# Kernel tuning notes

Measured on AMD Instinct MI355X. Metric: run time of the kernel, lower is better.

## Reference

```python
import jax, jax.numpy as jnp
import numpy as np

EPS = 1e-8
MARGIN = 0.2
LAMBDA_SM_LSE = 6.0   # i2t attention smooth (opt.lambda_softmax_lse)
LAMBDA_SM_AVG = 9.0   # t2i attention smooth (opt.lambda_softmax_avg)
LAMBDA_LSE = 6.0      # LogSumExp aggregation temperature
NEG = -1e9


def _l2norm(x, axis):
    return x / (jnp.sqrt(jnp.sum(x * x, axis=axis, keepdims=True)) + EPS)


def _cos(a, b):
    # cosine over last axis, torch-style: w12 / clamp(|a||b|, eps)
    w12 = jnp.sum(a * b, axis=-1)
    w1 = jnp.sqrt(jnp.sum(a * a, axis=-1))
    w2 = jnp.sqrt(jnp.sum(b * b, axis=-1))
    return w12 / jnp.maximum(w1 * w2, EPS)


def _forward(im, s, s_l):
    B, R, D = im.shape
    W = s.shape[1]
    wmask = jnp.arange(W)[None, :] < s_l[:, None]          # (Bc, W) valid words
    s = s * wmask[:, :, None]                              # emulate ragged slice s[j,:len_j]

    # ---------------- i2t: query=image regions, context=caption words ----------
    # attn[i,j,w,r] = <s[j,w], im[i,r]>
    A = jnp.einsum('jwd,ird->ijwr', s, im)
    A = jax.nn.leaky_relu(A, 0.1)
    A = _l2norm(A, axis=3)                                 # clipped_l2norm over regions
    logits = jnp.swapaxes(A, 2, 3) * LAMBDA_SM_LSE         # (i,j,r,w), softmax over words
    logits = jnp.where(wmask[None, :, None, :], logits, NEG)
    attn_i2t = jax.nn.softmax(logits, axis=-1)
    wc_t = jnp.einsum('ijrw,jwd->ijrd', attn_i2t, s)       # weighted caption ctx per region
    sim1 = _cos(im[:, None, :, :], wc_t)                   # (i,j,r)
    score1 = jnp.log(jnp.sum(jnp.exp(LAMBDA_LSE * sim1), axis=2)) / LAMBDA_LSE  # (i,j)
    attn_t_full = jnp.mean(wc_t, axis=2)                   # (i,j,d)
    idx = jnp.arange(B)
    attn_t = attn_t_full[idx, idx]                         # (B,d) diagonal

    # ---------------- t2i: query=caption words, context=image regions ----------
    # attn[i,j,r,w] = <im[i,r], s[j,w]>
    Bm = jnp.einsum('ird,jwd->ijrw', im, s)
    Bm = jax.nn.leaky_relu(Bm, 0.1)
    Bm = Bm * wmask[None, :, None, :]                      # padded-word cols excluded from norm
    Bm = _l2norm(Bm, axis=3)                               # clipped_l2norm over words
    logits2 = jnp.swapaxes(Bm, 2, 3) * LAMBDA_SM_AVG       # (i,j,w,r), softmax over regions
    attn_t2i = jax.nn.softmax(logits2, axis=-1)
    wc_i = jnp.einsum('ijwr,ird->ijwd', attn_t2i, im)      # weighted image ctx per word
    sim2 = _cos(s[None, :, :, :], wc_i)                    # (i,j,w)
    e2 = jnp.where(wmask[None, :, :], jnp.exp(LAMBDA_LSE * sim2), 0.0)
    score2 = jnp.log(jnp.sum(e2, axis=2)) / LAMBDA_LSE     # masked LogSumExp over words
    wsum = jnp.sum(wc_i * wmask[None, :, :, None], axis=2)
    attn_i_full = wsum / s_l[None, :, None].astype(wc_i.dtype)  # masked mean over words
    attn_i = attn_i_full[idx, idx]                         # (B,d)

    # ---------------- hinge loss over (B,B) score matrix -----------------------
    scores = 0.5 * (score1 + score2)
    diag = jnp.diagonal(scores)
    cost_s = jnp.maximum(MARGIN + scores - diag[:, None], 0.0)
    cost_im = jnp.maximum(MARGIN + scores - diag[None, :], 0.0)
    eye = jnp.eye(B, dtype=bool)
    cost_s = jnp.where(eye, 0.0, cost_s)
    cost_im = jnp.where(eye, 0.0, cost_im)
    # max_violation=True
    loss = jnp.sum(jnp.max(cost_s, axis=1)) + jnp.sum(jnp.max(cost_im, axis=0))
    return loss, attn_t, attn_i


def setup_inputs() -> dict:
    key = jax.random.key(0)
    k1, k2, k3 = jax.random.split(key, 3)
    B, R, W, D = 64, 36, 40, 1024
    im = jax.random.normal(k1, (B, R, D), dtype=jnp.float32)
    s = jax.random.normal(k2, (B, W, D), dtype=jnp.float32)
    s_l = jax.random.randint(k3, (B,), 10, W + 1)
    return {"im": im, "s": s, "s_l": s_l}


def reference(im, s, s_l):
    return _forward(im, s, s_l)
```

## Files before the change

kernel.cpp:

```cpp
#include <hip/hip_runtime.h>
#include <math.h>

#define Bn 64
#define Rr 36
#define Ww 40
#define Dd 1024
#define GM 2304
#define GN 2560
#define GLP 44
#define EPSf 1e-8f

typedef unsigned short u16;
typedef __attribute__((ext_vector_type(8))) short bf16x8;
typedef __attribute__((ext_vector_type(4))) float f32x4;

struct alignas(8) U16x4 { u16 x, y, z, w; };

__device__ inline u16 f2bf(float x) {
    unsigned int u = __float_as_uint(x);
    u += 0x7FFFu + ((u >> 16) & 1u);
    return (u16)(u >> 16);
}
__device__ inline float bf2f(u16 h) {
    return __uint_as_float(((unsigned int)h) << 16);
}

__device__ __forceinline__ void gl_lds16(const u16* g, u16* l) {
    __builtin_amdgcn_global_load_lds(
        (const __attribute__((address_space(1))) void*)g,
        (__attribute__((address_space(3))) void*)l, 16, 0, 0);
}

__global__ __launch_bounds__(256) void convert_kernel(const float* __restrict__ im,
                                                      const float* __restrict__ s,
                                                      const int* __restrict__ s_l,
                                                      u16* __restrict__ Ab,
                                                      u16* __restrict__ Bb) {
    const int nA4 = GM * Dd / 4;
    const int nB4 = GN * Dd / 4;
    int idx = blockIdx.x * 256 + threadIdx.x;
    if (idx < nA4) {
        float4 v = *(const float4*)(im + (size_t)idx * 4);
        U16x4 o = {f2bf(v.x), f2bf(v.y), f2bf(v.z), f2bf(v.w)};
        *(U16x4*)(Ab + (size_t)idx * 4) = o;
    } else if (idx < nA4 + nB4) {
        int i2 = idx - nA4;
        int f = i2 * 4;
        int row = f >> 10;
        int j = row / Ww, w = row - j * Ww;
        U16x4 o = {0, 0, 0, 0};
        if (w < s_l[j]) {
            float4 v = *(const float4*)(s + (size_t)f);
            o.x = f2bf(v.x); o.y = f2bf(v.y); o.z = f2bf(v.z); o.w = f2bf(v.w);
        }
        *(U16x4*)(Bb + (size_t)i2 * 4) = o;
    }
}

__global__ __launch_bounds__(256) void gram_mfma_kernel(const u16* __restrict__ Ab,
                                                        const u16* __restrict__ Bb,
                                                        float* __restrict__ SS,
                                                        float* __restrict__ II) {
    int b = blockIdx.x;
    bool isS = b < Bn;
    int idx = isS ? b : b - Bn;
    int n = isS ? Ww : Rr;
    const u16* base = isS ? (Bb + (size_t)idx * Ww * Dd) : (Ab + (size_t)idx * Rr * Dd);
    float* outp = isS ? (SS + (size_t)idx * Ww * Ww) : (II + (size_t)idx * Rr * Rr);
    int t = threadIdx.x, lane = t & 63, wid = t >> 6;
    int frow = lane & 15, fk = (lane >> 4) * 8;
    __shared__ float red[3][64][37];

    f32x4 acc[3][3];
    for (int m = 0; m < 3; ++m)
        for (int p = 0; p < 3; ++p) acc[m][p] = (f32x4){0.f, 0.f, 0.f, 0.f};

    for (int ks = 0; ks < 8; ++ks) {
        int k0 = wid * 256 + ks * 32;
        bf16x8 f[3];
        for (int m = 0; m < 3; ++m)
            f[m] = *(const bf16x8*)(base + (size_t)(m * 16 + frow) * Dd + k0 + fk);
        for (int m = 0; m < 3; ++m)
            for (int p = 0; p < 3; ++p)
                acc[m][p] = __builtin_amdgcn_mfma_f32_16x16x32_bf16(f[m], f[p], acc[m][p], 0, 0, 0);
    }
    if (wid) {
        for (int m = 0; m < 3; ++m)
            for (int p = 0; p < 3; ++p)
                for (int q = 0; q < 4; ++q)
                    red[wid - 1][lane][(m * 3 + p) * 4 + q] = acc[m][p][q];
    }
    __syncthreads();
    if (wid == 0) {
        for (int wv = 0; wv < 3; ++wv)
            for (int m = 0; m < 3; ++m)
                for (int p = 0; p < 3; ++p)
                    for (int q = 0; q < 4; ++q)
                        acc[m][p][q] += red[wv][lane][(m * 3 + p) * 4 + q];
        int crow = (lane >> 4) * 4, ccol = lane & 15;
        for (int m = 0; m < 3; ++m)
            for (int p = 0; p < 3; ++p)
                for (int q = 0; q < 4; ++q) {
                    int row = m * 16 + crow + q;
                    int col = p * 16 + ccol;
                    if (row < n && col < n) outp[row * n + col] = acc[m][p][q];
                }
    }
}

template <bool GB>
__global__ __launch_bounds__(256) void gemm_mfma_kernel(const u16* __restrict__ Ab,
                                                        const u16* __restrict__ Bb,
                                                        void* __restrict__ Gv) {
    __shared__ __align__(16) u16 As[2][64][64];
    __shared__ __align__(16) u16 Bs[2][128][64];
    int bn = blockIdx.x;
    int bm = blockIdx.y;
    int t = threadIdx.x;
    int lane = t & 63, wid = t >> 6;
    int wr = wid >> 1, wc = wid & 1;

    int lrow8 = lane >> 3;
    int sslot = (lane & 7) ^ lrow8;
    const u16* ga = Ab + ((size_t)(bm * 64 + wid * 16) + lrow8) * Dd + sslot * 8;
    const u16* gb = Bb + ((size_t)(bn * 128 + wid * 32) + lrow8) * Dd + sslot * 8;

    f32x4 acc[2][4];
    for (int m = 0; m < 2; ++m)
        for (int n = 0; n < 4; ++n) acc[m][n] = (f32x4){0.f, 0.f, 0.f, 0.f};

    int frow = lane & 15;
    int cgr = lane >> 4;

#define STAGE(BI, KK) do { \
        gl_lds16(ga + (KK), &As[BI][wid * 16][0]); \
        gl_lds16(ga + (size_t)8 * Dd + (KK), &As[BI][wid * 16 + 8][0]); \
        gl_lds16(gb + (KK), &Bs[BI][wid * 32][0]); \
        gl_lds16(gb + (size_t)8 * Dd + (KK), &Bs[BI][wid * 32 + 8][0]); \
        gl_lds16(gb + (size_t)16 * Dd + (KK), &Bs[BI][wid * 32 + 16][0]); \
        gl_lds16(gb + (size_t)24 * Dd + (KK), &Bs[BI][wid * 32 + 24][0]); \
    } while (0)

    STAGE(0, 0);
    for (int step = 0; step < 16; ++step) {
        int cur = step & 1;
        __syncthreads();
        if (step < 15) STAGE(cur ^ 1, (step + 1) * 64);
        bf16x8 af[2][2], bf[4][2];
#pragma unroll
        for (int m = 0; m < 2; ++m) {
            int row = wr * 32 + m * 16 + frow;
#pragma unroll
            for (int ks = 0; ks < 2; ++ks) {
                int slot = (ks * 4 + cgr) ^ (row & 7);
                af[m][ks] = *(const bf16x8*)&As[cur][row][slot * 8];
            }
        }
#pragma unroll
        for (int n = 0; n < 4; ++n) {
            int row = wc * 64 + n * 16 + frow;
#pragma unroll
            for (int ks = 0; ks < 2; ++ks) {
                int slot = (ks * 4 + cgr) ^ (row & 7);
                bf[n][ks] = *(const bf16x8*)&Bs[cur][row][slot * 8];
            }
        }
#pragma unroll
        for (int ks = 0; ks < 2; ++ks)
#pragma unroll
            for (int m = 0; m < 2; ++m)
#pragma unroll
                for (int n = 0; n < 4; ++n)
                    acc[m][n] = __builtin_amdgcn_mfma_f32_16x16x32_bf16(af[m][ks], bf[n][ks], acc[m][n], 0, 0, 0);
    }
#undef STAGE

    int crow0 = bm * 64 + wr * 32 + (lane >> 4) * 4;
    int ccol0 = bn * 128 + wc * 64 + (lane & 15);
    for (int m = 0; m < 2; ++m)
        for (int q = 0; q < 4; ++q) {
            int row = crow0 + m * 16 + q;
            for (int n = 0; n < 4; ++n) {
                float v = acc[m][n][q];
                size_t off = (size_t)row * GN + ccol0 + n * 16;
                if (GB) ((u16*)Gv)[off] = f2bf(v);
                else ((float*)Gv)[off] = v;
            }
        }
}

template <bool GB>
__global__ __launch_bounds__(128) void pair_kernel(const void* __restrict__ Gv,
                                                   const float* __restrict__ SS,
                                                   const float* __restrict__ II,
                                                   const int* __restrict__ s_l,
                                                   float* __restrict__ score1,
                                                   float* __restrict__ score2,
                                                   float* __restrict__ dAp,
                                                   float* __restrict__ dBp) {
    int j = blockIdx.x, i = blockIdx.y;
    int t = threadIdx.x, lane = t & 63, wid = t >> 6;
    __shared__ __align__(16) u16 glb[Rr * GLP];
    __shared__ __align__(16) u16 attA[Ww * Rr];
    __shared__ __align__(16) u16 attB[Rr * Ww];
    __shared__ float invA[Ww], invB[Rr], sA[Rr], sB[Ww];
    __shared__ float qpA[360], qpB[360];
    int L = s_l[j];
    float iid = 0.f, ssd = 0.f;

    if (wid == 0) {
        if (lane < Rr) {
            iid = II[(size_t)i * Rr * Rr + lane * (Rr + 1)];
            if (GB) {
                const u16* gp = (const u16*)Gv + (size_t)(i * Rr + lane) * GN + j * Ww;
#pragma unroll
                for (int q = 0; q < 10; ++q)
                    *(uint2*)&glb[lane * GLP + q * 4] = *(const uint2*)(gp + q * 4);
            } else {
                const float* gp = (const float*)Gv + (size_t)(i * Rr + lane) * GN + j * Ww;
#pragma unroll
                for (int q = 0; q < 10; ++q) {
                    float4 v = *(const float4*)(gp + q * 4);
                    U16x4 h = {f2bf(v.x), f2bf(v.y), f2bf(v.z), f2bf(v.w)};
                    *(uint2*)&glb[lane * GLP + q * 4] = *(const uint2*)&h;
                }
            }
            float sum = 0.f;
#pragma unroll 8
            for (int w = 0; w < Ww; ++w) {
                float x = bf2f(glb[lane * GLP + w]);
                x = x < 0.f ? 0.1f * x : x;
                sum += x * x;
            }
            invB[lane] = 9.f / (sqrtf(sum) + EPSf);
        }
    } else {
        if (lane < Ww) ssd = SS[(size_t)j * Ww * Ww + lane * (Ww + 1)];
    }
    __syncthreads();
    if (wid == 1 && lane < Ww) {
        float sum = 0.f;
#pragma unroll 6
        for (int r = 0; r < Rr; ++r) {
            float x = bf2f(glb[r * GLP + lane]);
            x = x < 0.f ? 0.1f * x : x;
            sum += x * x;
        }
        invA[lane] = 6.f / (sqrtf(sum) + EPSf);
    }
    __syncthreads();
    if (wid == 0) {
        float dot = 0.f, myinv = 0.f;
        if (lane < Rr) {
            float ssum = 0.f;
#pragma unroll 8
            for (int w = 0; w < Ww; ++w) {
                float e = 0.f;
                if (w < L) {
                    float gx = bf2f(glb[lane * GLP + w]);
                    float x = gx < 0.f ? 0.1f * gx : gx;
                    e = __expf(x * invA[w]);
                    dot += e * gx;
                }
                attA[w * Rr + lane] = f2bf(e);
                ssum += e;
            }
            myinv = 1.f / ssum;
            dot *= myinv;
            sA[lane] = myinv;
        }
#pragma unroll
        for (int rd = 0; rd < 2; ++rd) {
            int job = lane + rd * 64;
            if (job < 90) {
                int wg = job / 9, rg = job - (job / 9) * 9;
                float a4[4][4];
#pragma unroll
                for (int x = 0; x < 4; ++x)
#pragma unroll
                    for (int y = 0; y < 4; ++y) a4[x][y] = 0.f;
                const float* SSp = SS + (size_t)j * Ww * Ww + wg * 4;
#pragma unroll 4
                for (int w = 0; w < Ww; ++w) {
                    ushort4 a16 = *(const ushort4*)&attA[w * Rr + rg * 4];
                    float4 sv = *(const float4*)(SSp + w * Ww);
                    float av0 = bf2f(a16.x), av1 = bf2f(a16.y), av2 = bf2f(a16.z), av3 = bf2f(a16.w);
                    a4[0][0] += av0 * sv.x; a4[0][1] += av0 * sv.y; a4[0][2] += av0 * sv.z; a4[0][3] += av0 * sv.w;
                    a4[1][0] += av1 * sv.x; a4[1][1] += av1 * sv.y; a4[1][2] += av1 * sv.z; a4[1][3] += av1 * sv.w;
                    a4[2][0] += av2 * sv.x; a4[2][1] += av2 * sv.y; a4[2][2] += av2 * sv.z; a4[2][3] += av2 * sv.w;
                    a4[3][0] += av3 * sv.x; a4[3][1] += av3 * sv.y; a4[3][2] += av3 * sv.z; a4[3][3] += av3 * sv.w;
                }
                float qv0 = 0.f, qv1 = 0.f, qv2 = 0.f, qv3 = 0.f;
#pragma unroll
                for (int wj = 0; wj < 4; ++wj) {
                    ushort4 b16 = *(const ushort4*)&attA[(wg * 4 + wj) * Rr + rg * 4];
                    qv0 += bf2f(b16.x) * a4[0][wj];
                    qv1 += bf2f(b16.y) * a4[1][wj];
                    qv2 += bf2f(b16.z) * a4[2][wj];
                    qv3 += bf2f(b16.w) * a4[3][wj];
                }
                qpA[(rg * 4 + 0) * 10 + wg] = qv0;
                qpA[(rg * 4 + 1) * 10 + wg] = qv1;
                qpA[(rg * 4 + 2) * 10 + wg] = qv2;
                qpA[(rg * 4 + 3) * 10 + wg] = qv3;
            }
        }
        float e1 = 0.f;
        if (lane < Rr) {
            float q = 0.f;
#pragma unroll
            for (int wg = 0; wg < 10; ++wg) q += qpA[lane * 10 + wg];
            q *= myinv * myinv;
            float s1 = dot / fmaxf(sqrtf(iid) * sqrtf(fmaxf(q, 0.f)), EPSf);
            e1 = __expf(6.f * s1);
        }
#pragma unroll
        for (int off = 1; off < 64; off <<= 1) e1 += __shfl_xor(e1, off);
        if (lane == 0) score1[i * Bn + j] = __logf(e1) * (1.f / 6.f);
        if (i == j && lane < Ww) {
            float sum = 0.f;
#pragma unroll 6
            for (int r = 0; r < Rr; ++r) sum += bf2f(attA[lane * Rr + r]) * sA[r];
            dAp[i * Ww + lane] = sum * (1.f / (float)Rr);
        }
    } else {
        float dot = 0.f, myinv = 0.f;
        if (lane < Ww) {
            float ssum = 0.f;
#pragma unroll 6
            for (int r = 0; r < Rr; ++r) {
                float gx = bf2f(glb[r * GLP + lane]);
                float x = gx < 0.f ? 0.1f * gx : gx;
                float e = __expf(x * invB[r]);
                dot += e * gx;
                attB[r * Ww + lane] = f2bf(e);
                ssum += e;
            }
            myinv = 1.f / ssum;
            dot *= myinv;
            sB[lane] = myinv;
        }
#pragma unroll
        for (int rd = 0; rd < 2; ++rd) {
            int job = lane + rd * 64;
            if (job < 90) {
                int rg = job / 10, wg = job - (job / 10) * 10;
                float a4[4][4];
#pragma unroll
                for (int x = 0; x < 4; ++x)
#pragma unroll
                    for (int y = 0; y < 4; ++y) a4[x][y] = 0.f;
                const float* IIp = II + (size_t)i * Rr * Rr + rg * 4;
#pragma unroll 4
                for (int r = 0; r < Rr; ++r) {
                    ushort4 b16 = *(const ushort4*)&attB[r * Ww + wg * 4];
                    float4 iv = *(const float4*)(IIp + r * Rr);
                    float bv0 = bf2f(b16.x), bv1 = bf2f(b16.y), bv2 = bf2f(b16.z), bv3 = bf2f(b16.w);
                    a4[0][0] += bv0 * iv.x; a4[0][1] += bv0 * iv.y; a4[0][2] += bv0 * iv.z; a4[0][3] += bv0 * iv.w;
                    a4[1][0] += bv1 * iv.x; a4[1][1] += bv1 * iv.y; a4[1][2] += bv1 * iv.z; a4[1][3] += bv1 * iv.w;
                    a4[2][0] += bv2 * iv.x; a4[2][1] += bv2 * iv.y; a4[2][2] += bv2 * iv.z; a4[2][3] += bv2 * iv.w;
                    a4[3][0] += bv3 * iv.x; a4[3][1] += bv3 * iv.y; a4[3][2] += bv3 * iv.z; a4[3][3] += bv3 * iv.w;
                }
                float qv0 = 0.f, qv1 = 0.f, qv2 = 0.f, qv3 = 0.f;
#pragma unroll
                for (int rj = 0; rj < 4; ++rj) {
                    ushort4 b2 = *(const ushort4*)&attB[(rg * 4 + rj) * Ww + wg * 4];
                    qv0 += bf2f(b2.x) * a4[0][rj];
                    qv1 += bf2f(b2.y) * a4[1][rj];
                    qv2 += bf2f(b2.z) * a4[2][rj];
                    qv3 += bf2f(b2.w) * a4[3][rj];
                }
                qpB[(wg * 4 + 0) * 9 + rg] = qv0;
                qpB[(wg * 4 + 1) * 9 + rg] = qv1;
                qpB[(wg * 4 + 2) * 9 + rg] = qv2;
                qpB[(wg * 4 + 3) * 9 + rg] = qv3;
            }
        }
        float e2 = 0.f;
        if (lane < Ww) {
            float q = 0.f;
#pragma unroll
            for (int rg = 0; rg < 9; ++rg) q += qpB[lane * 9 + rg];
            q *= myinv * myinv;
            float s2 = dot / fmaxf(sqrtf(ssd) * sqrtf(fmaxf(q, 0.f)), EPSf);
            e2 = (lane < L) ? __expf(6.f * s2) : 0.f;
        }
#pragma unroll
        for (int off = 1; off < 64; off <<= 1) e2 += __shfl_xor(e2, off);
        if (lane == 0) score2[i * Bn + j] = __logf(e2) * (1.f / 6.f);
        if (i == j && lane < Rr) {
            float sum = 0.f;
            for (int w = 0; w < L; ++w) sum += bf2f(attB[lane * Ww + w]) * sB[w];
            dBp[i * Rr + lane] = sum / (float)L;
        }
    }
}

__global__ __launch_bounds__(256) void diag_out_kernel(const u16* __restrict__ Ab,
                                                       const u16* __restrict__ Bb,
                                                       const int* __restrict__ s_l,
                                                       const float* __restrict__ dA,
                                                       const float* __restrict__ dB,
                                                       const float* __restrict__ score1,
                                                       const float* __restrict__ score2,
                                                       float* __restrict__ out) {
    int t = threadIdx.x;
    if (blockIdx.y == 4) {
        if (blockIdx.x != 0) return;
        __shared__ float sc[Bn][Bn + 1];
        for (int idx = t; idx < Bn * Bn; idx += 256)
            sc[idx >> 6][idx & 63] = 0.5f * (score1[idx] + score2[idx]);
        __syncthreads();
        if (t < 64) {
            float dt = sc[t][t];
            float rowmax = 0.f, colmax = 0.f;
            for (int k = 0; k < Bn; ++k) {
                if (k != t) {
                    rowmax = fmaxf(rowmax, 0.2f + sc[t][k] - dt);
                    colmax = fmaxf(colmax, 0.2f + sc[k][t] - dt);
                }
            }
            float v = rowmax + colmax;
            for (int off = 32; off; off >>= 1) v += __shfl_down(v, off);
            if (t == 0) out[0] = v;
        }
        return;
    }
    int i = blockIdx.x;
    int d = blockIdx.y * 256 + t;
    int L = s_l[i];
    __shared__ float aw[Ww], br[Rr];
    if (t < Ww) aw[t] = dA[i * Ww + t];
    if (t >= 64 && t < 64 + Rr) br[t - 64] = dB[i * Rr + (t - 64)];
    __syncthreads();
    float acc1 = 0.f;
    for (int w = 0; w < L; ++w) acc1 += aw[w] * bf2f(Bb[((size_t)i * Ww + w) * Dd + d]);
    out[1 + (size_t)i * Dd + d] = acc1;
    float acc2 = 0.f;
    for (int r = 0; r < Rr; ++r) acc2 += br[r] * bf2f(Ab[((size_t)i * Rr + r) * Dd + d]);
    out[1 + (size_t)Bn * Dd + (size_t)i * Dd + d] = acc2;
}

extern "C" void kernel_launch(void* const* d_in, const int* in_sizes, int n_in,
                              void* d_out, int out_size, void* d_ws, size_t ws_size,
                              hipStream_t stream) {
    const float* im = (const float*)d_in[0];
    const float* s = (const float*)d_in[1];
    const int* s_l = (const int*)d_in[2];
    float* out = (float*)d_out;

    const size_t nAb = (size_t)GM * Dd;
    const size_t nBb = (size_t)GN * Dd;
    u16* Ab = (u16*)d_ws;
    u16* Bb = Ab + nAb;
    float* SS = (float*)(Bb + nBb);
    float* II = SS + (size_t)Bn * Ww * Ww;
    float* score1 = II + (size_t)Bn * Rr * Rr;
    float* score2 = score1 + Bn * Bn;
    float* dA = score2 + Bn * Bn;
    float* dB = dA + Bn * Ww;
    void* G = (void*)(dB + Bn * Rr);
    size_t base_bytes = (char*)G - (char*)d_ws;
    bool g_fp32 = (ws_size >= base_bytes + (size_t)GM * GN * 4);

    int nconv = (GM * Dd + GN * Dd) / 4;
    convert_kernel<<<(nconv + 255) / 256, 256, 0, stream>>>(im, s, s_l, Ab, Bb);
    gram_mfma_kernel<<<2 * Bn, 256, 0, stream>>>(Ab, Bb, SS, II);

    dim3 ggrid(GN / 128, GM / 64);
    dim3 pgrid(Bn, Bn);
    if (g_fp32) {
        gemm_mfma_kernel<false><<<ggrid, 256, 0, stream>>>(Ab, Bb, G);
        pair_kernel<false><<<pgrid, 128, 0, stream>>>(G, SS, II, s_l, score1, score2, dA, dB);
    } else {
        gemm_mfma_kernel<true><<<ggrid, 256, 0, stream>>>(Ab, Bb, G);
        pair_kernel<true><<<pgrid, 128, 0, stream>>>(G, SS, II, s_l, score1, score2, dA, dB);
    }

    dim3 dgrid(Bn, 5);
    diag_out_kernel<<<dgrid, 256, 0, stream>>>(Ab, Bb, s_l, dA, dB, score1, score2, out);
}
```

Baseline: 79.37 us.

## Fuse pairwise GEMM into per-pair attention kernel and merge convert with Gram

Measured after the change: 147.4 us. +85.7%, slower.

```diff
diff --git a/kernel.cpp b/kernel.cpp
--- a/kernel.cpp
+++ b/kernel.cpp
@@ -7,7 +7,8 @@
 #define Dd 1024
 #define GM 2304
 #define GN 2560
-#define GLP 44
+#define GP 41
+#define NCONV 4864
 #define EPSf 1e-8f
 
 typedef unsigned short u16;
@@ -25,61 +26,65 @@
     return __uint_as_float(((unsigned int)h) << 16);
 }
 
-__device__ __forceinline__ void gl_lds16(const u16* g, u16* l) {
-    __builtin_amdgcn_global_load_lds(
-        (const __attribute__((address_space(1))) void*)g,
-        (__attribute__((address_space(3))) void*)l, 16, 0, 0);
-}
-
-__global__ __launch_bounds__(256) void convert_kernel(const float* __restrict__ im,
-                                                      const float* __restrict__ s,
-                                                      const int* __restrict__ s_l,
-                                                      u16* __restrict__ Ab,
-                                                      u16* __restrict__ Bb) {
-    const int nA4 = GM * Dd / 4;
-    const int nB4 = GN * Dd / 4;
-    int idx = blockIdx.x * 256 + threadIdx.x;
-    if (idx < nA4) {
-        float4 v = *(const float4*)(im + (size_t)idx * 4);
-        U16x4 o = {f2bf(v.x), f2bf(v.y), f2bf(v.z), f2bf(v.w)};
-        *(U16x4*)(Ab + (size_t)idx * 4) = o;
-    } else if (idx < nA4 + nB4) {
-        int i2 = idx - nA4;
-        int f = i2 * 4;
-        int row = f >> 10;
-        int j = row / Ww, w = row - j * Ww;
-        U16x4 o = {0, 0, 0, 0};
-        if (w < s_l[j]) {
-            float4 v = *(const float4*)(s + (size_t)f);
-            o.x = f2bf(v.x); o.y = f2bf(v.y); o.z = f2bf(v.z); o.w = f2bf(v.w);
-        }
-        *(U16x4*)(Bb + (size_t)i2 * 4) = o;
-    }
-}
-
-__global__ __launch_bounds__(256) void gram_mfma_kernel(const u16* __restrict__ Ab,
-                                                        const u16* __restrict__ Bb,
-                                                        float* __restrict__ SS,
-                                                        float* __restrict__ II) {
-    int b = blockIdx.x;
-    bool isS = b < Bn;
-    int idx = isS ? b : b - Bn;
+__global__ __launch_bounds__(256) void prep_kernel(const float* __restrict__ im,
+                                                   const float* __restrict__ s,
+                                                   const int* __restrict__ s_l,
+                                                   u16* __restrict__ Ab,
+                                                   u16* __restrict__ Bb,
+                                                   float* __restrict__ SS,
+                                                   float* __restrict__ II) {
+    __shared__ float red[3][64][37];
+    int b = blockIdx.x, t = threadIdx.x;
+    if (b < NCONV) {
+        const int nA4 = GM * Dd / 4;
+        int idx = b * 256 + t;
+        if (idx < nA4) {
+            float4 v = *(const float4*)(im + (size_t)idx * 4);
+            U16x4 o = {f2bf(v.x), f2bf(v.y), f2bf(v.z), f2bf(v.w)};
+            *(U16x4*)(Ab + (size_t)idx * 4) = o;
+        } else {
+            int i2 = idx - nA4;
+            int f = i2 * 4;
+            int row = f >> 10;
+            int j = row / Ww, w = row - j * Ww;
+            U16x4 o = {0, 0, 0, 0};
+            if (w < s_l[j]) {
+                float4 v = *(const float4*)(s + (size_t)f);
+                o.x = f2bf(v.x); o.y = f2bf(v.y); o.z = f2bf(v.z); o.w = f2bf(v.w);
+            }
+            *(U16x4*)(Bb + (size_t)i2 * 4) = o;
+        }
+        return;
+    }
+    int gb = b - NCONV;
+    bool isS = gb < Bn;
+    int idx = isS ? gb : gb - Bn;
     int n = isS ? Ww : Rr;
-    const u16* base = isS ? (Bb + (size_t)idx * Ww * Dd) : (Ab + (size_t)idx * Rr * Dd);
+    const float* basef = isS ? (s + (size_t)idx * Ww * Dd) : (im + (size_t)idx * Rr * Dd);
     float* outp = isS ? (SS + (size_t)idx * Ww * Ww) : (II + (size_t)idx * Rr * Rr);
-    int t = threadIdx.x, lane = t & 63, wid = t >> 6;
+    int lane = t & 63, wid = t >> 6;
     int frow = lane & 15, fk = (lane >> 4) * 8;
-    __shared__ float red[3][64][37];
 
     f32x4 acc[3][3];
     for (int m = 0; m < 3; ++m)
         for (int p = 0; p < 3; ++p) acc[m][p] = (f32x4){0.f, 0.f, 0.f, 0.f};
 
     for (int ks = 0; ks < 8; ++ks) {
-        int k0 = wid * 256 + ks * 32;
+        int k0 = wid * 256 + ks * 32 + fk;
         bf16x8 f[3];
-        for (int m = 0; m < 3; ++m)
-            f[m] = *(const bf16x8*)(base + (size_t)(m * 16 + frow) * Dd + k0 + fk);
+        for (int m = 0; m < 3; ++m) {
+            int rr = m * 16 + frow;
+            if (rr >= n) rr = n - 1;
+            const float* p = basef + (size_t)rr * Dd + k0;
+            float4 v0 = *(const float4*)p;
+            float4 v1 = *(const float4*)(p + 4);
+            bf16x8 fv;
+            fv[0] = (short)f2bf(v0.x); fv[1] = (short)f2bf(v0.y);
+            fv[2] = (short)f2bf(v0.z); fv[3] = (short)f2bf(v0.w);
+            fv[4] = (short)f2bf(v1.x); fv[5] = (short)f2bf(v1.y);
+            fv[6] = (short)f2bf(v1.z); fv[7] = (short)f2bf(v1.w);
+            f[m] = fv;
+        }
         for (int m = 0; m < 3; ++m)
             for (int p = 0; p < 3; ++p)
                 acc[m][p] = __builtin_amdgcn_mfma_f32_16x16x32_bf16(f[m], f[p], acc[m][p], 0, 0, 0);
@@ -108,203 +113,188 @@
     }
 }
 
-template <bool GB>
-__global__ __launch_bounds__(256) void gemm_mfma_kernel(const u16* __restrict__ Ab,
-                                                        const u16* __restrict__ Bb,
-                                                        void* __restrict__ Gv) {
-    __shared__ __align__(16) u16 As[2][64][64];
-    __shared__ __align__(16) u16 Bs[2][128][64];
-    int bn = blockIdx.x;
-    int bm = blockIdx.y;
-    int t = threadIdx.x;
-    int lane = t & 63, wid = t >> 6;
-    int wr = wid >> 1, wc = wid & 1;
-
-    int lrow8 = lane >> 3;
-    int sslot = (lane & 7) ^ lrow8;
-    const u16* ga = Ab + ((size_t)(bm * 64 + wid * 16) + lrow8) * Dd + sslot * 8;
-    const u16* gb = Bb + ((size_t)(bn * 128 + wid * 32) + lrow8) * Dd + sslot * 8;
-
-    f32x4 acc[2][4];
-    for (int m = 0; m < 2; ++m)
-        for (int n = 0; n < 4; ++n) acc[m][n] = (f32x4){0.f, 0.f, 0.f, 0.f};
-
-    int frow = lane & 15;
-    int cgr = lane >> 4;
-
-#define STAGE(BI, KK) do { \
-        gl_lds16(ga + (KK), &As[BI][wid * 16][0]); \
-        gl_lds16(ga + (size_t)8 * Dd + (KK), &As[BI][wid * 16 + 8][0]); \
-        gl_lds16(gb + (KK), &Bs[BI][wid * 32][0]); \
-        gl_lds16(gb + (size_t)8 * Dd + (KK), &Bs[BI][wid * 32 + 8][0]); \
-        gl_lds16(gb + (size_t)16 * Dd + (KK), &Bs[BI][wid * 32 + 16][0]); \
-        gl_lds16(gb + (size_t)24 * Dd + (KK), &Bs[BI][wid * 32 + 24][0]); \
-    } while (0)
-
-    STAGE(0, 0);
-    for (int step = 0; step < 16; ++step) {
-        int cur = step & 1;
-        __syncthreads();
-        if (step < 15) STAGE(cur ^ 1, (step + 1) * 64);
-        bf16x8 af[2][2], bf[4][2];
-#pragma unroll
-        for (int m = 0; m < 2; ++m) {
-            int row = wr * 32 + m * 16 + frow;
-#pragma unroll
-            for (int ks = 0; ks < 2; ++ks) {
-                int slot = (ks * 4 + cgr) ^ (row & 7);
-                af[m][ks] = *(const bf16x8*)&As[cur][row][slot * 8];
-            }
-        }
-#pragma unroll
-        for (int n = 0; n < 4; ++n) {
-            int row = wc * 64 + n * 16 + frow;
-#pragma unroll
-            for (int ks = 0; ks < 2; ++ks) {
-                int slot = (ks * 4 + cgr) ^ (row & 7);
-                bf[n][ks] = *(const bf16x8*)&Bs[cur][row][slot * 8];
-            }
-        }
-#pragma unroll
-        for (int ks = 0; ks < 2; ++ks)
-#pragma unroll
-            for (int m = 0; m < 2; ++m)
-#pragma unroll
-                for (int n = 0; n < 4; ++n)
-                    acc[m][n] = __builtin_amdgcn_mfma_f32_16x16x32_bf16(af[m][ks], bf[n][ks], acc[m][n], 0, 0, 0);
-    }
-#undef STAGE
-
-    int crow0 = bm * 64 + wr * 32 + (lane >> 4) * 4;
-    int ccol0 = bn * 128 + wc * 64 + (lane & 15);
-    for (int m = 0; m < 2; ++m)
-        for (int q = 0; q < 4; ++q) {
-            int row = crow0 + m * 16 + q;
-            for (int n = 0; n < 4; ++n) {
-                float v = acc[m][n][q];
-                size_t off = (size_t)row * GN + ccol0 + n * 16;
-                if (GB) ((u16*)Gv)[off] = f2bf(v);
-                else ((float*)Gv)[off] = v;
-            }
-        }
-}
-
-template <bool GB>
-__global__ __launch_bounds__(128) void pair_kernel(const void* __restrict__ Gv,
-                                                   const float* __restrict__ SS,
-                                                   const float* __restrict__ II,
-                                                   const int* __restrict__ s_l,
-                                                   float* __restrict__ score1,
-                                                   float* __restrict__ score2,
-                                                   float* __restrict__ dAp,
-                                                   float* __restrict__ dBp) {
+__global__ __launch_bounds__(256) void fused_kernel(const u16* __restrict__ Ab,
+                                                    const u16* __restrict__ Bb,
+                                                    const float* __restrict__ SS,
+                                                    const float* __restrict__ II,
+                                                    const int* __restrict__ s_l,
+                                                    float* __restrict__ score1,
+                                                    float* __restrict__ score2,
+                                                    float* __restrict__ dAp,
+                                                    float* __restrict__ dBp) {
     int j = blockIdx.x, i = blockIdx.y;
     int t = threadIdx.x, lane = t & 63, wid = t >> 6;
-    __shared__ __align__(16) u16 glb[Rr * GLP];
+    __shared__ __align__(16) float gacc[Rr * GP];
     __shared__ __align__(16) u16 attA[Ww * Rr];
     __shared__ __align__(16) u16 attB[Rr * Ww];
     __shared__ float invA[Ww], invB[Rr], sA[Rr], sB[Ww];
-    __shared__ float qpA[360], qpB[360];
+    __shared__ __align__(16) float qpA[360], qpB[360];
     int L = s_l[j];
+
     float iid = 0.f, ssd = 0.f;
-
-    if (wid == 0) {
-        if (lane < Rr) {
-            iid = II[(size_t)i * Rr * Rr + lane * (Rr + 1)];
-            if (GB) {
-                const u16* gp = (const u16*)Gv + (size_t)(i * Rr + lane) * GN + j * Ww;
-#pragma unroll
-                for (int q = 0; q < 10; ++q)
-                    *(uint2*)&glb[lane * GLP + q * 4] = *(const uint2*)(gp + q * 4);
-            } else {
-                const float* gp = (const float*)Gv + (size_t)(i * Rr + lane) * GN + j * Ww;
-#pragma unroll
-                for (int q = 0; q < 10; ++q) {
-                    float4 v = *(const float4*)(gp + q * 4);
-                    U16x4 h = {f2bf(v.x), f2bf(v.y), f2bf(v.z), f2bf(v.w)};
-                    *(uint2*)&glb[lane * GLP + q * 4] = *(const uint2*)&h;
-                }
-            }
-            float sum = 0.f;
-#pragma unroll 8
-            for (int w = 0; w < Ww; ++w) {
-                float x = bf2f(glb[lane * GLP + w]);
-                x = x < 0.f ? 0.1f * x : x;
-                sum += x * x;
-            }
-            invB[lane] = 9.f / (sqrtf(sum) + EPSf);
-        }
-    } else {
-        if (lane < Ww) ssd = SS[(size_t)j * Ww * Ww + lane * (Ww + 1)];
-    }
-    __syncthreads();
+    if (wid == 0 && lane < Rr) iid = II[(size_t)i * Rr * Rr + lane * (Rr + 1)];
+    if (wid == 1 && lane < Ww) ssd = SS[(size_t)j * Ww * Ww + lane * (Ww + 1)];
+
+    const u16* Abase = Ab + (size_t)(i * Rr) * Dd;
+    const u16* Bbase = Bb + (size_t)(j * Ww) * Dd;
+    int frow = lane & 15, fk = (lane >> 4) * 8;
+    f32x4 acc[3][3];
+    for (int m = 0; m < 3; ++m)
+        for (int p = 0; p < 3; ++p) acc[m][p] = (f32x4){0.f, 0.f, 0.f, 0.f};
+#pragma unroll
+    for (int ks = 0; ks < 8; ++ks) {
+        int k0 = wid * 256 + ks * 32 + fk;
+        bf16x8 fa[3], fb[3];
+#pragma unroll
+        for (int m = 0; m < 3; ++m)
+            fa[m] = *(const bf16x8*)(Abase + (size_t)(m * 16 + frow) * Dd + k0);
+#pragma unroll
+        for (int p = 0; p < 3; ++p)
+            fb[p] = *(const bf16x8*)(Bbase + (size_t)(p * 16 + frow) * Dd + k0);
+#pragma unroll
+        for (int m = 0; m < 3; ++m)
+#pragma unroll
+            for (int p = 0; p < 3; ++p)
+                acc[m][p] = __builtin_amdgcn_mfma_f32_16x16x32_bf16(fa[m], fb[p], acc[m][p], 0, 0, 0);
+    }
+    int crow = (lane >> 4) * 4, ccol = lane & 15;
+    for (int wv = 0; wv < 4; ++wv) {
+        if (wid == wv) {
+            for (int m = 0; m < 3; ++m)
+                for (int p = 0; p < 3; ++p)
+                    for (int q = 0; q < 4; ++q) {
+                        int r = m * 16 + crow + q, w = p * 16 + ccol;
+                        if (r < Rr && w < Ww) {
+                            if (wv == 0) gacc[r * GP + w] = acc[m][p][q];
+                            else gacc[r * GP + w] += acc[m][p][q];
+                        }
+                    }
+        }
+        __syncthreads();
+    }
     if (wid == 1 && lane < Ww) {
         float sum = 0.f;
 #pragma unroll 6
         for (int r = 0; r < Rr; ++r) {
-            float x = bf2f(glb[r * GLP + lane]);
+            float x = gacc[r * GP + lane];
             x = x < 0.f ? 0.1f * x : x;
             sum += x * x;
         }
         invA[lane] = 6.f / (sqrtf(sum) + EPSf);
     }
+    if (wid == 0 && lane < Rr) {
+        float sum = 0.f;
+#pragma unroll 8
+        for (int w = 0; w < Ww; ++w) {
+            float x = gacc[lane * GP + w];
+            x = x < 0.f ? 0.1f * x : x;
+            sum += x * x;
+        }
+        invB[lane] = 9.f / (sqrtf(sum) + EPSf);
+    }
+    __syncthreads();
+    float dot = 0.f, myinv = 0.f;
+    if (wid == 0 && lane < Rr) {
+        float ssum = 0.f;
+#pragma unroll 8
+        for (int w = 0; w < Ww; ++w) {
+            float e = 0.f;
+            if (w < L) {
+                float gx = gacc[lane * GP + w];
+                float x = gx < 0.f ? 0.1f * gx : gx;
+                e = __expf(x * invA[w]);
+                dot += e * gx;
+            }
+            attA[w * Rr + lane] = f2bf(e);
+            ssum += e;
+        }
+        myinv = 1.f / ssum;
+        dot *= myinv;
+        sA[lane] = myinv;
+    }
+    if (wid == 1 && lane < Ww) {
+        float ssum = 0.f;
+#pragma unroll 6
+        for (int r = 0; r < Rr; ++r) {
+            float gx = gacc[r * GP + lane];
+            float x = gx < 0.f ? 0.1f * gx : gx;
+            float e = __expf(x * invB[lane == lane ? r : r]);
+            e = __expf(x * invB[r]);
+            dot += e * gx;
+            attB[r * Ww + lane] = f2bf(e);
+            ssum += e;
+        }
+        myinv = 1.f / ssum;
+        dot *= myinv;
+        sB[lane] = myinv;
+    }
+    __syncthreads();
+    if (t < 90) {
+        int wg = t / 9, rg = t - wg * 9;
+        float a4[4][4];
+#pragma unroll
+        for (int x = 0; x < 4; ++x)
+#pragma unroll
+            for (int y = 0; y < 4; ++y) a4[x][y] = 0.f;
+        const float* SSp = SS + (size_t)j * Ww * Ww + wg * 4;
+#pragma unroll 4
+        for (int w = 0; w < Ww; ++w) {
+            ushort4 a16 = *(const ushort4*)&attA[w * Rr + rg * 4];
+            float4 sv = *(const float4*)(SSp + (size_t)w * Ww);
+            float av0 = bf2f(a16.x), av1 = bf2f(a16.y), av2 = bf2f(a16.z), av3 = bf2f(a16.w);
+            a4[0][0] += av0 * sv.x; a4[0][1] += av0 * sv.y; a4[0][2] += av0 * sv.z; a4[0][3] += av0 * sv.w;
+            a4[1][0] += av1 * sv.x; a4[1][1] += av1 * sv.y; a4[1][2] += av1 * sv.z; a4[1][3] += av1 * sv.w;
+            a4[2][0] += av2 * sv.x; a4[2][1] += av2 * sv.y; a4[2][2] += av2 * sv.z; a4[2][3] += av2 * sv.w;
+            a4[3][0] += av3 * sv.x; a4[3][1] += av3 * sv.y; a4[3][2] += av3 * sv.z; a4[3][3] += av3 * sv.w;
+        }
+        float qv0 = 0.f, qv1 = 0.f, qv2 = 0.f, qv3 = 0.f;
+#pragma unroll
+        for (int wj = 0; wj < 4; ++wj) {
+            ushort4 b16 = *(const ushort4*)&attA[(wg * 4 + wj) * Rr + rg * 4];
+            qv0 += bf2f(b16.x) * a4[0][wj];
+            qv1 += bf2f(b16.y) * a4[1][wj];
+            qv2 += bf2f(b16.z) * a4[2][wj];
+            qv3 += bf2f(b16.w) * a4[3][wj];
+        }
+        qpA[(rg * 4 + 0) * 10 + wg] = qv0;
+        qpA[(rg * 4 + 1) * 10 + wg] = qv1;
+        qpA[(rg * 4 + 2) * 10 + wg] = qv2;
+        qpA[(rg * 4 + 3) * 10 + wg] = qv3;
+    } else if (t >= 128 && t < 218) {
+        int job = t - 128;
+        int rg = job / 10, wg = job - rg * 10;
+        float a4[4][4];
+#pragma unroll
+        for (int x = 0; x < 4; ++x)
+#pragma unroll
+            for (int y = 0; y < 4; ++y) a4[x][y] = 0.f;
+        const float* IIp = II + (size_t)i * Rr * Rr + rg * 4;
+#pragma unroll 4
+        for (int r = 0; r < Rr; ++r) {
+            ushort4 b16 = *(const ushort4*)&attB[r * Ww + wg * 4];
+            float4 iv = *(const float4*)(IIp + (size_t)r * Rr);
+            float bv0 = bf2f(b16.x), bv1 = bf2f(b16.y), bv2 = bf2f(b16.z), bv3 = bf2f(b16.w);
+            a4[0][0] += bv0 * iv.x; a4[0][1] += bv0 * iv.y; a4[0][2] += bv0 * iv.z; a4[0][3] += bv0 * iv.w;
+            a4[1][0] += bv1 * iv.x; a4[1][1] += bv1 * iv.y; a4[1][2] += bv1 * iv.z; a4[1][3] += bv1 * iv.w;
+            a4[2][0] += bv2 * iv.x; a4[2][1] += bv2 * iv.y; a4[2][2] += bv2 * iv.z; a4[2][3] += bv2 * iv.w;
+            a4[3][0] += bv3 * iv.x; a4[3][1] += bv3 * iv.y; a4[3][2] += bv3 * iv.z; a4[3][3] += bv3 * iv.w;
+        }
+        float qv0 = 0.f, qv1 = 0.f, qv2 = 0.f, qv3 = 0.f;
+#pragma unroll
+        for (int rj = 0; rj < 4; ++rj) {
+            ushort4 b2 = *(const ushort4*)&attB[(rg * 4 + rj) * Ww + wg * 4];
+            qv0 += bf2f(b2.x) * a4[0][rj];
+            qv1 += bf2f(b2.y) * a4[1][rj];
+            qv2 += bf2f(b2.z) * a4[2][rj];
+            qv3 += bf2f(b2.w) * a4[3][rj];
+        }
+        qpB[(wg * 4 + 0) * 9 + rg] = qv0;
+        qpB[(wg * 4 + 1) * 9 + rg] = qv1;
+        qpB[(wg * 4 + 2) * 9 + rg] = qv2;
+        qpB[(wg * 4 + 3) * 9 + rg] = qv3;
+    }
     __syncthreads();
     if (wid == 0) {
-        float dot = 0.f, myinv = 0.f;
-        if (lane < Rr) {
-            float ssum = 0.f;
-#pragma unroll 8
-            for (int w = 0; w < Ww; ++w) {
-                float e = 0.f;
-                if (w < L) {
-                    float gx = bf2f(glb[lane * GLP + w]);
-                    float x = gx < 0.f ? 0.1f * gx : gx;
-                    e = __expf(x * invA[w]);
-                    dot += e * gx;
-                }
-                attA[w * Rr + lane] = f2bf(e);
-                ssum += e;
-            }
-            myinv = 1.f / ssum;
-            dot *= myinv;
-            sA[lane] = myinv;
-        }
-#pragma unroll
-        for (int rd = 0; rd < 2; ++rd) {
-            int job = lane + rd * 64;
-            if (job < 90) {
-                int wg = job / 9, rg = job - (job / 9) * 9;
-                float a4[4][4];
-#pragma unroll
-                for (int x = 0; x < 4; ++x)
-#pragma unroll
-                    for (int y = 0; y < 4; ++y) a4[x][y] = 0.f;
-                const float* SSp = SS + (size_t)j * Ww * Ww + wg * 4;
-#pragma unroll 4
-                for (int w = 0; w < Ww; ++w) {
-                    ushort4 a16 = *(const ushort4*)&attA[w * Rr + rg * 4];
-                    float4 sv = *(const float4*)(SSp + w * Ww);
-                    float av0 = bf2f(a16.x), av1 = bf2f(a16.y), av2 = bf2f(a16.z), av3 = bf2f(a16.w);
-                    a4[0][0] += av0 * sv.x; a4[0][1] += av0 * sv.y; a4[0][2] += av0 * sv.z; a4[0][3] += av0 * sv.w;
-                    a4[1][0] += av1 * sv.x; a4[1][1] += av1 * sv.y; a4[1][2] += av1 * sv.z; a4[1][3] += av1 * sv.w;
-                    a4[2][0] += av2 * sv.x; a4[2][1] += av2 * sv.y; a4[2][2] += av2 * sv.z; a4[2][3] += av2 * sv.w;
-                    a4[3][0] += av3 * sv.x; a4[3][1] += av3 * sv.y; a4[3][2] += av3 * sv.z; a4[3][3] += av3 * sv.w;
-                }
-                float qv0 = 0.f, qv1 = 0.f, qv2 = 0.f, qv3 = 0.f;
-#pragma unroll
-                for (int wj = 0; wj < 4; ++wj) {
-                    ushort4 b16 = *(const ushort4*)&attA[(wg * 4 + wj) * Rr + rg * 4];
-                    qv0 += bf2f(b16.x) * a4[0][wj];
-                    qv1 += bf2f(b16.y) * a4[1][wj];
-                    qv2 += bf2f(b16.z) * a4[2][wj];
-                    qv3 += bf2f(b16.w) * a4[3][wj];
-                }
-                qpA[(rg * 4 + 0) * 10 + wg] = qv0;
-                qpA[(rg * 4 + 1) * 10 + wg] = qv1;
-                qpA[(rg * 4 + 2) * 10 + wg] = qv2;
-                qpA[(rg * 4 + 3) * 10 + wg] = qv3;
-            }
-        }
         float e1 = 0.f;
         if (lane < Rr) {
             float q = 0.f;
@@ -317,78 +307,26 @@
 #pragma unroll
         for (int off = 1; off < 64; off <<= 1) e1 += __shfl_xor(e1, off);
         if (lane == 0) score1[i * Bn + j] = __logf(e1) * (1.f / 6.f);
-        if (i == j && lane < Ww) {
+    } else if (wid == 1) {
+        float e2 = 0.f;
+        if (lane < Ww) {
+            float q = 0.f;
+#pragma unroll
+            for (int rg = 0; rg < 9; ++rg) q += qpB[lane * 9 + rg];
+            q *= myinv * myinv;
+            float s2 = dot / fmaxf(sqrtf(ssd) * sqrtf(fmaxf(q, 0.f)), EPSf);
+            e2 = (lane < L) ? __expf(6.f * s2) : 0.f;
+        }
+#pragma unroll
+        for (int off = 1; off < 64; off <<= 1) e2 += __shfl_xor(e2, off);
+        if (lane == 0) score2[i * Bn + j] = __logf(e2) * (1.f / 6.f);
+    } else if (i == j) {
+        if (wid == 2 && lane < Ww) {
             float sum = 0.f;
 #pragma unroll 6
             for (int r = 0; r < Rr; ++r) sum += bf2f(attA[lane * Rr + r]) * sA[r];
             dAp[i * Ww + lane] = sum * (1.f / (float)Rr);
-        }
-    } else {
-        float dot = 0.f, myinv = 0.f;
-        if (lane < Ww) {
-            float ssum = 0.f;
-#pragma unroll 6
-            for (int r = 0; r < Rr; ++r) {
-                float gx = bf2f(glb[r * GLP + lane]);
-                float x = gx < 0.f ? 0.1f * gx : gx;
-                float e = __expf(x * invB[r]);
-                dot += e * gx;
-                attB[r * Ww + lane] = f2bf(e);
-                ssum += e;
-            }
-            myinv = 1.f / ssum;
-            dot *= myinv;
-            sB[lane] = myinv;
-        }
-#pragma unroll
-        for (int rd = 0; rd < 2; ++rd) {
-            int job = lane + rd * 64;
-            if (job < 90) {
-                int rg = job / 10, wg = job - (job / 10) * 10;
-                float a4[4][4];
-#pragma unroll
-                for (int x = 0; x < 4; ++x)
-#pragma unroll
-                    for (int y = 0; y < 4; ++y) a4[x][y] = 0.f;
-                const float* IIp = II + (size_t)i * Rr * Rr + rg * 4;
-#pragma unroll 4
-                for (int r = 0; r < Rr; ++r) {
-                    ushort4 b16 = *(const ushort4*)&attB[r * Ww + wg * 4];
-                    float4 iv = *(const float4*)(IIp + r * Rr);
-                    float bv0 = bf2f(b16.x), bv1 = bf2f(b16.y), bv2 = bf2f(b16.z), bv3 = bf2f(b16.w);
-                    a4[0][0] += bv0 * iv.x; a4[0][1] += bv0 * iv.y; a4[0][2] += bv0 * iv.z; a4[0][3] += bv0 * iv.w;
-                    a4[1][0] += bv1 * iv.x; a4[1][1] += bv1 * iv.y; a4[1][2] += bv1 * iv.z; a4[1][3] += bv1 * iv.w;
-                    a4[2][0] += bv2 * iv.x; a4[2][1] += bv2 * iv.y; a4[2][2] += bv2 * iv.z; a4[2][3] += bv2 * iv.w;
-                    a4[3][0] += bv3 * iv.x; a4[3][1] += bv3 * iv.y; a4[3][2] += bv3 * iv.z; a4[3][3] += bv3 * iv.w;
-                }
-                float qv0 = 0.f, qv1 = 0.f, qv2 = 0.f, qv3 = 0.f;
-#pragma unroll
-                for (int rj = 0; rj < 4; ++rj) {
-                    ushort4 b2 = *(const ushort4*)&attB[(rg * 4 + rj) * Ww + wg * 4];
-                    qv0 += bf2f(b2.x) * a4[0][rj];
-                    qv1 += bf2f(b2.y) * a4[1][rj];
-                    qv2 += bf2f(b2.z) * a4[2][rj];
-                    qv3 += bf2f(b2.w) * a4[3][rj];
-                }
-                qpB[(wg * 4 + 0) * 9 + rg] = qv0;
-                qpB[(wg * 4 + 1) * 9 + rg] = qv1;
-                qpB[(wg * 4 + 2) * 9 + rg] = qv2;
-                qpB[(wg * 4 + 3) * 9 + rg] = qv3;
-            }
-        }
-        float e2 = 0.f;
-        if (lane < Ww) {
-            float q = 0.f;
-#pragma unroll
-            for (int rg = 0; rg < 9; ++rg) q += qpB[lane * 9 + rg];
-            q *= myinv * myinv;
-            float s2 = dot / fmaxf(sqrtf(ssd) * sqrtf(fmaxf(q, 0.f)), EPSf);
-            e2 = (lane < L) ? __expf(6.f * s2) : 0.f;
-        }
-#pragma unroll
-        for (int off = 1; off < 64; off <<= 1) e2 += __shfl_xor(e2, off);
-        if (lane == 0) score2[i * Bn + j] = __logf(e2) * (1.f / 6.f);
-        if (i == j && lane < Rr) {
+        } else if (wid == 3 && lane < Rr) {
             float sum = 0.f;
             for (int w = 0; w < L; ++w) sum += bf2f(attB[lane * Ww + w]) * sB[w];
             dBp[i * Rr + lane] = sum / (float)L;
@@ -459,23 +397,11 @@
     float* score2 = score1 + Bn * Bn;
     float* dA = score2 + Bn * Bn;
     float* dB = dA + Bn * Ww;
-    void* G = (void*)(dB + Bn * Rr);
-    size_t base_bytes = (char*)G - (char*)d_ws;
-    bool g_fp32 = (ws_size >= base_bytes + (size_t)GM * GN * 4);
-
-    int nconv = (GM * Dd + GN * Dd) / 4;
-    convert_kernel<<<(nconv + 255) / 256, 256, 0, stream>>>(im, s, s_l, Ab, Bb);
-    gram_mfma_kernel<<<2 * Bn, 256, 0, stream>>>(Ab, Bb, SS, II);
-
-    dim3 ggrid(GN / 128, GM / 64);
-    dim3 pgrid(Bn, Bn);
-    if (g_fp32) {
-        gemm_mfma_kernel<false><<<ggrid, 256, 0, stream>>>(Ab, Bb, G);
-        pair_kernel<false><<<pgrid, 128, 0, stream>>>(G, SS, II, s_l, score1, score2, dA, dB);
-    } else {
-        gemm_mfma_kernel<true><<<ggrid, 256, 0, stream>>>(Ab, Bb, G);
-        pair_kernel<true><<<pgrid, 128, 0, stream>>>(G, SS, II, s_l, score1, score2, dA, dB);
-    }
+
+    prep_kernel<<<NCONV + 2 * Bn, 256, 0, stream>>>(im, s, s_l, Ab, Bb, SS, II);
+
+    dim3 fgrid(Bn, Bn);
+    fused_kernel<<<fgrid, 256, 0, stream>>>(Ab, Bb, SS, II, s_l, score1, score2, dA, dB);
 
     dim3 dgrid(Bn, 5);
     diag_out_kernel<<<dgrid, 256, 0, stream>>>(Ab, Bb, s_l, dA, dB, score1, score2, out);
```
